# Kernel tuning notes

Measured on AMD Instinct MI355X. Metric: run time of the kernel, lower is better.

## Reference

```python
import jax, jax.numpy as jnp
import numpy as np

N_NODES = 50000
N_EDGES = 800000
F_IN = 128
HID = 128
N_CLASSES = 12
N_GRAPHS = 128


def setup_inputs() -> dict:
    key = jax.random.key(0)
    ks = jax.random.split(key, 12)
    x = jax.random.normal(ks[0], (N_NODES, F_IN), dtype=jnp.float32)
    edge_index = jax.random.randint(ks[1], (2, N_EDGES), 0, N_NODES, dtype=jnp.int64)
    batch = jnp.sort(jax.random.randint(ks[2], (N_NODES,), 0, N_GRAPHS, dtype=jnp.int64))
    def glorot(k, fan_in, fan_out):
        s = jnp.sqrt(6.0 / (fan_in + fan_out))
        return jax.random.uniform(k, (fan_in, fan_out), jnp.float32, -s, s)
    return {
        "x": x,
        "edge_index": edge_index,
        "batch": batch,
        "W0": glorot(ks[3], F_IN, HID), "b0": jnp.zeros((HID,), jnp.float32),
        "W1": glorot(ks[4], HID, HID), "b1": jnp.zeros((HID,), jnp.float32),
        "W2": glorot(ks[5], HID, HID), "b2": jnp.zeros((HID,), jnp.float32),
        "lin_w": glorot(ks[6], HID, N_CLASSES),
        "lin_b": jnp.zeros((N_CLASSES,), jnp.float32),
    }


def _gcn_norm(edge_index, n_nodes):
    # add self loops then compute symmetric normalization D^-1/2 (A+I) D^-1/2
    loops = jnp.arange(n_nodes, dtype=edge_index.dtype)
    row = jnp.concatenate([edge_index[0], loops])
    col = jnp.concatenate([edge_index[1], loops])
    deg = jax.ops.segment_sum(jnp.ones_like(col, dtype=jnp.float32), col, num_segments=n_nodes)
    dis = jnp.where(deg > 0, jax.lax.rsqrt(deg), 0.0)
    norm = dis[row] * dis[col]  # [E + N]
    return row, col, norm


def _gcn_conv(x, W, b, row, col, norm, n_nodes):
    xw = x @ W                                   # [N, H] dense GEMM
    msg = xw[row] * norm[:, None]                # gather + scale [E+N, H]
    out = jax.ops.segment_sum(msg, col, num_segments=n_nodes)  # scatter-add
    return out + b


def reference(x, edge_index, batch, W0, b0, W1, b1, W2, b2, lin_w, lin_b):
    n = x.shape[0]
    row, col, norm = _gcn_norm(edge_index, n)
    h = x
    for W, b in ((W0, b0), (W1, b1), (W2, b2)):
        h = jax.nn.relu(_gcn_conv(h, W, b, row, col, norm, n))
        # dropout is identity in eval mode
    # global mean pool over graphs
    sums = jax.ops.segment_sum(h, batch, num_segments=N_GRAPHS)        # [G, H]
    cnt = jax.ops.segment_sum(jnp.ones((n,), h.dtype), batch, num_segments=N_GRAPHS)
    pooled = sums / jnp.maximum(cnt, 1.0)[:, None]
    return pooled @ lin_w + lin_b  # [G, C]
```

## Files before the change

### kernel.cpp

```cpp
#include <hip/hip_runtime.h>
#include <hip/hip_bf16.h>

#define HID 128
#define NCLS 12
#define NGRAPH 128

typedef __attribute__((ext_vector_type(8))) short short8v;
typedef __attribute__((ext_vector_type(4))) float float4v;

__device__ __forceinline__ ushort f2bf(float f) {
    uint u = __float_as_uint(f);
    u += 0x7FFFu + ((u >> 16) & 1u);
    return (ushort)(u >> 16);
}
__device__ __forceinline__ float bf2f(ushort u) {
    return __uint_as_float(((uint)u) << 16);
}
__device__ __forceinline__ float4 bf4tof(ushort4 u) {
    float4 f;
    f.x = bf2f(u.x); f.y = bf2f(u.y); f.z = bf2f(u.z); f.w = bf2f(u.w);
    return f;
}


__global__ void hist_kernel(const int* __restrict__ ei, int* __restrict__ cnt, int E) {
    int e = blockIdx.x * blockDim.x + threadIdx.x;
    if (e < E) {
        int c = ei[E + e];
        atomicAdd(&cnt[c], 1);
    }
}

__global__ void scan1_kernel(const int* __restrict__ cnt, int* __restrict__ offs,
                             int* __restrict__ bsum, float* __restrict__ dis, int n) {
    __shared__ int s[1024];
    int t = threadIdx.x;
    int v = blockIdx.x * 1024 + t;
    int val = (v < n) ? cnt[v] : 0;
    if (v < n) dis[v] = rsqrtf((float)(val + 1));
    s[t] = val;
    __syncthreads();
    for (int off = 1; off < 1024; off <<= 1) {
        int add = (t >= off) ? s[t - off] : 0;
        __syncthreads();
        s[t] += add;
        __syncthreads();
    }
    if (v < n) offs[v] = s[t] - val;
    if (t == 1023) bsum[blockIdx.x] = s[1023];
}

__global__ void scan2_kernel(const int* __restrict__ bsum, int* __restrict__ bscan, int nb) {
    if (threadIdx.x == 0 && blockIdx.x == 0) {
        int run = 0;
        for (int b = 0; b < nb; b++) { bscan[b] = run; run += bsum[b]; }
        bscan[nb] = run;
    }
}

__global__ void scan3_kernel(int* __restrict__ offs, int* __restrict__ cursor,
                             const int* __restrict__ bscan, int n, int E) {
    int v = blockIdx.x * blockDim.x + threadIdx.x;
    if (v < n) {
        int o = offs[v] + bscan[v >> 10];
        offs[v] = o;
        cursor[v] = o;
    }
    if (v == 0) offs[n] = E;
}

__global__ void fill_kernel(const int* __restrict__ ei, int* __restrict__ cursor,
                            int* __restrict__ srcs, int E) {
    int e = blockIdx.x * blockDim.x + threadIdx.x;
    if (e < E) {
        int r = ei[e];
        int c = ei[E + e];
        int p = atomicAdd(&cursor[c], 1);
        srcs[p] = r;
    }
}


__global__ void cvtx_kernel(const float* __restrict__ x, ushort* __restrict__ xb, int total) {
    int i = (blockIdx.x * blockDim.x + threadIdx.x) * 4;
    if (i < total) {
        float4 v = *(const float4*)&x[i];
        ushort4 o;
        o.x = f2bf(v.x); o.y = f2bf(v.y); o.z = f2bf(v.z); o.w = f2bf(v.w);
        *(ushort4*)&xb[i] = o;
    }
}

__global__ void cvtw_kernel(const float* __restrict__ W, ushort* __restrict__ Wt) {
    int idx = blockIdx.x * 256 + threadIdx.x;
    int k = idx >> 7;
    int c = idx & 127;
    Wt[c * HID + k] = f2bf(W[k * HID + c]);
}


__global__ __launch_bounds__(256) void gemm_bf16_kernel(
    const ushort* __restrict__ A, const ushort* __restrict__ Wt,
    const float* __restrict__ dis, ushort* __restrict__ Y, int n)
{
    int tid  = threadIdx.x;
    int wave = tid >> 6;
    int lane = tid & 63;
    int l15  = lane & 15;
    int lg   = lane >> 4;
    int rowbase = blockIdx.x * 128 + wave * 32;

    float4v acc[2][8];
#pragma unroll
    for (int m = 0; m < 2; m++)
#pragma unroll
        for (int nn = 0; nn < 8; nn++)
            acc[m][nn] = (float4v){0.f, 0.f, 0.f, 0.f};

#pragma unroll
    for (int kk = 0; kk < 4; kk++) {
        int k0 = kk * 32 + lg * 8;
        short8v a[2];
#pragma unroll
        for (int m = 0; m < 2; m++) {
            int row = rowbase + m * 16 + l15;
            if (row < n) a[m] = *(const short8v*)&A[row * HID + k0];
            else         a[m] = (short8v){0,0,0,0,0,0,0,0};
        }
        short8v b[8];
#pragma unroll
        for (int nn = 0; nn < 8; nn++)
            b[nn] = *(const short8v*)&Wt[(nn * 16 + l15) * HID + k0];
#pragma unroll
        for (int m = 0; m < 2; m++)
#pragma unroll
            for (int nn = 0; nn < 8; nn++)
                acc[m][nn] = __builtin_amdgcn_mfma_f32_16x16x32_bf16(
                    b[nn], a[m], acc[m][nn], 0, 0, 0);
    }

#pragma unroll
    for (int m = 0; m < 2; m++) {
        int row = rowbase + m * 16 + l15;
        if (row < n) {
            float d = dis[row];
#pragma unroll
            for (int nn = 0; nn < 8; nn++) {
                ushort4 o;
                o.x = f2bf(acc[m][nn][0] * d);
                o.y = f2bf(acc[m][nn][1] * d);
                o.z = f2bf(acc[m][nn][2] * d);
                o.w = f2bf(acc[m][nn][3] * d);
                *(ushort4*)&Y[row * HID + nn * 16 + lg * 4] = o;
            }
        }
    }
}


__global__ __launch_bounds__(256) void aggregate_bf16_kernel(
    const ushort* __restrict__ Y, const int* __restrict__ offs,
    const int* __restrict__ srcs, const float* __restrict__ dis,
    const float* __restrict__ bias, ushort* __restrict__ H, int n)
{
    int tid = threadIdx.x;
    int node = blockIdx.x * 8 + (tid >> 5);
    if (node >= n) return;
    int lane = tid & 31;
    int c = lane * 4;
    const ushort* Yc = Y + c;

    float4 a0 = bf4tof(*(const ushort4*)&Yc[node * HID]);
    float4 a1 = make_float4(0.f, 0.f, 0.f, 0.f);
    float4 a2 = make_float4(0.f, 0.f, 0.f, 0.f);
    float4 a3 = make_float4(0.f, 0.f, 0.f, 0.f);
    float4 a4 = make_float4(0.f, 0.f, 0.f, 0.f);
    float4 a5 = make_float4(0.f, 0.f, 0.f, 0.f);
    float4 a6 = make_float4(0.f, 0.f, 0.f, 0.f);
    float4 a7 = make_float4(0.f, 0.f, 0.f, 0.f);

    int beg = offs[node];
    int end = offs[node + 1];
    int j = beg;
    for (; j + 8 <= end; j += 8) {
        int r0 = srcs[j + 0], r1 = srcs[j + 1], r2 = srcs[j + 2], r3 = srcs[j + 3];
        int r4 = srcs[j + 4], r5 = srcs[j + 5], r6 = srcs[j + 6], r7 = srcs[j + 7];
        float4 v0 = bf4tof(*(const ushort4*)&Yc[r0 * HID]);
        float4 v1 = bf4tof(*(const ushort4*)&Yc[r1 * HID]);
        float4 v2 = bf4tof(*(const ushort4*)&Yc[r2 * HID]);
        float4 v3 = bf4tof(*(const ushort4*)&Yc[r3 * HID]);
        float4 v4 = bf4tof(*(const ushort4*)&Yc[r4 * HID]);
        float4 v5 = bf4tof(*(const ushort4*)&Yc[r5 * HID]);
        float4 v6 = bf4tof(*(const ushort4*)&Yc[r6 * HID]);
        float4 v7 = bf4tof(*(const ushort4*)&Yc[r7 * HID]);
        a0.x += v0.x; a0.y += v0.y; a0.z += v0.z; a0.w += v0.w;
        a1.x += v1.x; a1.y += v1.y; a1.z += v1.z; a1.w += v1.w;
        a2.x += v2.x; a2.y += v2.y; a2.z += v2.z; a2.w += v2.w;
        a3.x += v3.x; a3.y += v3.y; a3.z += v3.z; a3.w += v3.w;
        a4.x += v4.x; a4.y += v4.y; a4.z += v4.z; a4.w += v4.w;
        a5.x += v5.x; a5.y += v5.y; a5.z += v5.z; a5.w += v5.w;
        a6.x += v6.x; a6.y += v6.y; a6.z += v6.z; a6.w += v6.w;
        a7.x += v7.x; a7.y += v7.y; a7.z += v7.z; a7.w += v7.w;
    }
    for (; j + 2 <= end; j += 2) {
        int r0 = srcs[j + 0], r1 = srcs[j + 1];
        float4 v0 = bf4tof(*(const ushort4*)&Yc[r0 * HID]);
        float4 v1 = bf4tof(*(const ushort4*)&Yc[r1 * HID]);
        a0.x += v0.x; a0.y += v0.y; a0.z += v0.z; a0.w += v0.w;
        a1.x += v1.x; a1.y += v1.y; a1.z += v1.z; a1.w += v1.w;
    }
    if (j < end) {
        int r0 = srcs[j];
        float4 v0 = bf4tof(*(const ushort4*)&Yc[r0 * HID]);
        a0.x += v0.x; a0.y += v0.y; a0.z += v0.z; a0.w += v0.w;
    }

    a0.x += a1.x + a2.x + a3.x + a4.x + a5.x + a6.x + a7.x;
    a0.y += a1.y + a2.y + a3.y + a4.y + a5.y + a6.y + a7.y;
    a0.z += a1.z + a2.z + a3.z + a4.z + a5.z + a6.z + a7.z;
    a0.w += a1.w + a2.w + a3.w + a4.w + a5.w + a6.w + a7.w;

    float d = dis[node];
    float4 bb = *(const float4*)&bias[c];
    ushort4 o;
    o.x = f2bf(fmaxf(fmaf(d, a0.x, bb.x), 0.f));
    o.y = f2bf(fmaxf(fmaf(d, a0.y, bb.y), 0.f));
    o.z = f2bf(fmaxf(fmaf(d, a0.z, bb.z), 0.f));
    o.w = f2bf(fmaxf(fmaf(d, a0.w, bb.w), 0.f));
    *(ushort4*)&H[node * HID + c] = o;
}


__global__ __launch_bounds__(256) void pool_kernel(
    const ushort* __restrict__ H, const int* __restrict__ batch,
    float* __restrict__ gsum, float* __restrict__ gcnt, int n)
{
    int half = blockIdx.x * 8 + (threadIdx.x >> 5);
    int lane = threadIdx.x & 31;
    int c = lane * 4;
    int n0 = half * 16;
    if (n0 >= n) return;
    int n1 = min(n0 + 16, n);

    float4 acc = make_float4(0.f, 0.f, 0.f, 0.f);
    float cntv = 0.f;
    int gprev = batch[n0];
    for (int v = n0; v < n1; v++) {
        int g = batch[v];
        if (g != gprev) {
            atomicAdd(&gsum[gprev * HID + c + 0], acc.x);
            atomicAdd(&gsum[gprev * HID + c + 1], acc.y);
            atomicAdd(&gsum[gprev * HID + c + 2], acc.z);
            atomicAdd(&gsum[gprev * HID + c + 3], acc.w);
            if (lane == 0) atomicAdd(&gcnt[gprev], cntv);
            acc = make_float4(0.f, 0.f, 0.f, 0.f);
            cntv = 0.f;
            gprev = g;
        }
        float4 h = bf4tof(*(const ushort4*)&H[v * HID + c]);
        acc.x += h.x; acc.y += h.y; acc.z += h.z; acc.w += h.w;
        cntv += 1.f;
    }
    atomicAdd(&gsum[gprev * HID + c + 0], acc.x);
    atomicAdd(&gsum[gprev * HID + c + 1], acc.y);
    atomicAdd(&gsum[gprev * HID + c + 2], acc.z);
    atomicAdd(&gsum[gprev * HID + c + 3], acc.w);
    if (lane == 0) atomicAdd(&gcnt[gprev], cntv);
}


__global__ __launch_bounds__(128) void classify_kernel(
    const float* __restrict__ gsum, const float* __restrict__ gcnt,
    const float* __restrict__ lin_w, const float* __restrict__ lin_b,
    float* __restrict__ out)
{
    __shared__ float sp[HID];
    int g = blockIdx.x;
    int f = threadIdx.x;
    float denom = fmaxf(gcnt[g], 1.0f);
    sp[f] = gsum[g * HID + f] / denom;
    __syncthreads();
    if (f < NCLS) {
        float acc = lin_b[f];
        for (int k = 0; k < HID; k++) acc = fmaf(sp[k], lin_w[k * NCLS + f], acc);
        out[g * NCLS + f] = acc;
    }
}


extern "C" void kernel_launch(void* const* d_in, const int* in_sizes, int n_in,
                              void* d_out, int out_size, void* d_ws, size_t ws_size,
                              hipStream_t stream) {
    const float* x     = (const float*)d_in[0];
    const int*   ei    = (const int*)d_in[1];
    const int*   batch = (const int*)d_in[2];
    const float* W0    = (const float*)d_in[3];
    const float* b0    = (const float*)d_in[4];
    const float* W1    = (const float*)d_in[5];
    const float* b1    = (const float*)d_in[6];
    const float* W2    = (const float*)d_in[7];
    const float* b2    = (const float*)d_in[8];
    const float* lin_w = (const float*)d_in[9];
    const float* lin_b = (const float*)d_in[10];
    float* out = (float*)d_out;

    const int n = in_sizes[0] / HID;
    const int E = in_sizes[1] / 2;

    char* w = (char*)d_ws;
    auto carve = [&](size_t bytes) {
        void* p = (void*)w;
        w += (bytes + 255) & ~(size_t)255;
        return p;
    };
    int*    cnt    = (int*)carve((size_t)n * 4);
    int*    offs   = (int*)carve(((size_t)n + 1) * 4);
    int*    cursor = (int*)carve((size_t)n * 4);
    int*    bsum   = (int*)carve(256 * 4);
    int*    bscan  = (int*)carve(256 * 4);
    int*    srcs   = (int*)carve((size_t)E * 4);
    float*  dis    = (float*)carve((size_t)n * 4);
    ushort* xb     = (ushort*)carve((size_t)n * HID * 2);
    ushort* Wt0    = (ushort*)carve((size_t)HID * HID * 2);
    ushort* Wt1    = (ushort*)carve((size_t)HID * HID * 2);
    ushort* Wt2    = (ushort*)carve((size_t)HID * HID * 2);
    ushort* Y      = (ushort*)carve((size_t)n * HID * 2);
    ushort* Hb     = (ushort*)carve((size_t)n * HID * 2);
    float*  gsum   = (float*)carve((size_t)NGRAPH * HID * 4);
    float*  gcnt   = (float*)carve((size_t)NGRAPH * 4);

    hipMemsetAsync(cnt, 0, (size_t)n * 4, stream);
    hipMemsetAsync(gsum, 0, (size_t)NGRAPH * HID * 4, stream);
    hipMemsetAsync(gcnt, 0, (size_t)NGRAPH * 4, stream);

    const int TB = 256;
    int gE = (E + TB - 1) / TB;
    int gN = (n + TB - 1) / TB;
    int nb1 = (n + 1023) / 1024;

    hist_kernel<<<gE, TB, 0, stream>>>(ei, cnt, E);
    scan1_kernel<<<nb1, 1024, 0, stream>>>(cnt, offs, bsum, dis, n);
    scan2_kernel<<<1, 64, 0, stream>>>(bsum, bscan, nb1);
    scan3_kernel<<<gN, TB, 0, stream>>>(offs, cursor, bscan, n, E);
    fill_kernel<<<gE, TB, 0, stream>>>(ei, cursor, srcs, E);

    int totalx = n * HID;
    cvtx_kernel<<<(totalx / 4 + TB - 1) / TB, TB, 0, stream>>>(x, xb, totalx);
    cvtw_kernel<<<64, 256, 0, stream>>>(W0, Wt0);
    cvtw_kernel<<<64, 256, 0, stream>>>(W1, Wt1);
    cvtw_kernel<<<64, 256, 0, stream>>>(W2, Wt2);

    int gGemm = (n + 127) / 128;
    int gAgg  = (n + 7) / 8;

    gemm_bf16_kernel<<<gGemm, TB, 0, stream>>>(xb, Wt0, dis, Y, n);
    aggregate_bf16_kernel<<<gAgg, TB, 0, stream>>>(Y, offs, srcs, dis, b0, Hb, n);
    gemm_bf16_kernel<<<gGemm, TB, 0, stream>>>(Hb, Wt1, dis, Y, n);
    aggregate_bf16_kernel<<<gAgg, TB, 0, stream>>>(Y, offs, srcs, dis, b1, Hb, n);
    gemm_bf16_kernel<<<gGemm, TB, 0, stream>>>(Hb, Wt2, dis, Y, n);
    aggregate_bf16_kernel<<<gAgg, TB, 0, stream>>>(Y, offs, srcs, dis, b2, Hb, n);

    int halves = (n + 15) / 16;
    int gPool = (halves + 7) / 8;
    pool_kernel<<<gPool, TB, 0, stream>>>(Hb, batch, gsum, gcnt, n);
    classify_kernel<<<NGRAPH, 128, 0, stream>>>(gsum, gcnt, lin_w, lin_b, out);
}
```

Measured before the change: 377.0 us.

## Build CSR via two-level bucket partition with shared-memory atomics

Replaces the five-kernel CSR build (global atomic histogram, three scan kernels, global atomic fill) with three kernels. Edges are first bucketed by destination block (256 nodes) per 4096-edge section in shared memory, then each block counts and places its own edges with shared-memory atomics. This removes heavy global atomic contention and several launches, at the cost of an intermediate int2 partition buffer. In csr_kernel each thread walks one section serially, so load balance depends on how edges are spread across sections, and edge order within a node changes.

```diff
diff --git a/kernel.cpp b/kernel.cpp
--- a/kernel.cpp
+++ b/kernel.cpp
@@ -4,6 +4,7 @@
 #define HID 128
 #define NCLS 12
 #define NGRAPH 128
+#define EPB 4096
 
 typedef __attribute__((ext_vector_type(8))) short short8v;
 typedef __attribute__((ext_vector_type(4))) float float4v;
@@ -23,60 +24,114 @@
 }
 
 
-__global__ void hist_kernel(const int* __restrict__ ei, int* __restrict__ cnt, int E) {
-    int e = blockIdx.x * blockDim.x + threadIdx.x;
-    if (e < E) {
-        int c = ei[E + e];
-        atomicAdd(&cnt[c], 1);
-    }
-}
-
-__global__ void scan1_kernel(const int* __restrict__ cnt, int* __restrict__ offs,
-                             int* __restrict__ bsum, float* __restrict__ dis, int n) {
-    __shared__ int s[1024];
+__global__ __launch_bounds__(256) void part_kernel(
+    const int* __restrict__ ei, int2* __restrict__ part,
+    int* __restrict__ lscan, int* __restrict__ btot, int E, int nb)
+{
+    __shared__ int h[256], sc[256], cur[256];
+    int k = blockIdx.x;
     int t = threadIdx.x;
-    int v = blockIdx.x * 1024 + t;
-    int val = (v < n) ? cnt[v] : 0;
-    if (v < n) dis[v] = rsqrtf((float)(val + 1));
-    s[t] = val;
-    __syncthreads();
-    for (int off = 1; off < 1024; off <<= 1) {
-        int add = (t >= off) ? s[t - off] : 0;
-        __syncthreads();
-        s[t] += add;
-        __syncthreads();
-    }
-    if (v < n) offs[v] = s[t] - val;
-    if (t == 1023) bsum[blockIdx.x] = s[1023];
-}
-
-__global__ void scan2_kernel(const int* __restrict__ bsum, int* __restrict__ bscan, int nb) {
-    if (threadIdx.x == 0 && blockIdx.x == 0) {
-        int run = 0;
-        for (int b = 0; b < nb; b++) { bscan[b] = run; run += bsum[b]; }
-        bscan[nb] = run;
-    }
-}
-
-__global__ void scan3_kernel(int* __restrict__ offs, int* __restrict__ cursor,
-                             const int* __restrict__ bscan, int n, int E) {
-    int v = blockIdx.x * blockDim.x + threadIdx.x;
-    if (v < n) {
-        int o = offs[v] + bscan[v >> 10];
-        offs[v] = o;
-        cursor[v] = o;
-    }
-    if (v == 0) offs[n] = E;
-}
-
-__global__ void fill_kernel(const int* __restrict__ ei, int* __restrict__ cursor,
-                            int* __restrict__ srcs, int E) {
-    int e = blockIdx.x * blockDim.x + threadIdx.x;
-    if (e < E) {
-        int r = ei[e];
-        int c = ei[E + e];
-        int p = atomicAdd(&cursor[c], 1);
-        srcs[p] = r;
+    int e0 = k * EPB, e1 = min(e0 + EPB, E);
+
+    h[t] = 0;
+    __syncthreads();
+    for (int e = e0 + t; e < e1; e += 256)
+        atomicAdd(&h[ei[E + e] >> 8], 1);
+    __syncthreads();
+
+    sc[t] = h[t];
+    __syncthreads();
+    for (int off = 1; off < 256; off <<= 1) {
+        int add = (t >= off) ? sc[t - off] : 0;
+        __syncthreads();
+        sc[t] += add;
+        __syncthreads();
+    }
+    int excl = sc[t] - h[t];
+    cur[t] = excl;
+    if (t < nb) {
+        lscan[k * (nb + 1) + t] = excl;
+        if (h[t] > 0) atomicAdd(&btot[t], h[t]);
+    }
+    if (t == 0) lscan[k * (nb + 1) + nb] = e1 - e0;
+    __syncthreads();
+
+    for (int e = e0 + t; e < e1; e += 256) {
+        int r = ei[e], c = ei[E + e];
+        int lr = atomicAdd(&cur[c >> 8], 1);
+        part[e0 + lr] = make_int2(r, c);
+    }
+}
+
+
+__global__ void gscan_kernel(const int* __restrict__ btot, int* __restrict__ gstart,
+                             int nb, int E) {
+    __shared__ int sc[256];
+    int t = threadIdx.x;
+    int v = (t < nb) ? btot[t] : 0;
+    sc[t] = v;
+    __syncthreads();
+    for (int off = 1; off < 256; off <<= 1) {
+        int add = (t >= off) ? sc[t - off] : 0;
+        __syncthreads();
+        sc[t] += add;
+        __syncthreads();
+    }
+    if (t < nb) gstart[t] = sc[t] - v;
+    if (t == 0) gstart[nb] = E;
+}
+
+
+__global__ __launch_bounds__(256) void csr_kernel(
+    const int2* __restrict__ part, const int* __restrict__ lscan,
+    const int* __restrict__ gstart, int* __restrict__ offs,
+    int* __restrict__ srcs, float* __restrict__ dis,
+    int n, int E, int nb, int nsec)
+{
+    __shared__ int cnt[256], sc[256], cur[256];
+    int b = blockIdx.x, t = threadIdx.x;
+
+    cnt[t] = 0;
+    __syncthreads();
+    for (int k = t; k < nsec; k += 256) {
+        const int* lrow = &lscan[k * (nb + 1)];
+        int s0 = lrow[b], s1 = lrow[b + 1];
+        int base = k * EPB;
+        for (int e = s0; e < s1; e++) {
+            int2 pr = part[base + e];
+            atomicAdd(&cnt[pr.y & 255], 1);
+        }
+    }
+    __syncthreads();
+
+    sc[t] = cnt[t];
+    __syncthreads();
+    for (int off = 1; off < 256; off <<= 1) {
+        int add = (t >= off) ? sc[t - off] : 0;
+        __syncthreads();
+        sc[t] += add;
+        __syncthreads();
+    }
+    int excl = sc[t] - cnt[t];
+    int g0 = gstart[b];
+    int d = b * 256 + t;
+    if (d < n) {
+        offs[d] = g0 + excl;
+        dis[d] = rsqrtf((float)(cnt[t] + 1));
+    }
+    cur[t] = g0 + excl;
+    if (b == nb - 1 && t == 0) offs[n] = E;
+    __syncthreads();
+
+    for (int k = t; k < nsec; k += 256) {
+        const int* lrow = &lscan[k * (nb + 1)];
+        int s0 = lrow[b], s1 = lrow[b + 1];
+        int base = k * EPB;
+        for (int e = s0; e < s1; e++) {
+            int2 pr = part[base + e];
+            int p = atomicAdd(&cur[pr.y & 255], 1);
+            srcs[p] = pr.x;
+        }
     }
 }
 
@@ -306,6 +361,8 @@
 
     const int n = in_sizes[0] / HID;
     const int E = in_sizes[1] / 2;
+    const int nb = (n + 255) / 256;
+    const int nsec = (E + EPB - 1) / EPB;
 
     char* w = (char*)d_ws;
     auto carve = [&](size_t bytes) {
@@ -313,11 +370,11 @@
         w += (bytes + 255) & ~(size_t)255;
         return p;
     };
-    int*    cnt    = (int*)carve((size_t)n * 4);
+    int2*   part   = (int2*)carve((size_t)E * 8);
+    int*    lscan  = (int*)carve((size_t)nsec * (nb + 1) * 4);
+    int*    btot   = (int*)carve((size_t)nb * 4);
+    int*    gstart = (int*)carve((size_t)(nb + 1) * 4);
     int*    offs   = (int*)carve(((size_t)n + 1) * 4);
-    int*    cursor = (int*)carve((size_t)n * 4);
-    int*    bsum   = (int*)carve(256 * 4);
-    int*    bscan  = (int*)carve(256 * 4);
     int*    srcs   = (int*)carve((size_t)E * 4);
     float*  dis    = (float*)carve((size_t)n * 4);
     ushort* xb     = (ushort*)carve((size_t)n * HID * 2);
@@ -329,20 +386,15 @@
     float*  gsum   = (float*)carve((size_t)NGRAPH * HID * 4);
     float*  gcnt   = (float*)carve((size_t)NGRAPH * 4);
 
-    hipMemsetAsync(cnt, 0, (size_t)n * 4, stream);
+    hipMemsetAsync(btot, 0, (size_t)nb * 4, stream);
     hipMemsetAsync(gsum, 0, (size_t)NGRAPH * HID * 4, stream);
     hipMemsetAsync(gcnt, 0, (size_t)NGRAPH * 4, stream);
 
     const int TB = 256;
-    int gE = (E + TB - 1) / TB;
-    int gN = (n + TB - 1) / TB;
-    int nb1 = (n + 1023) / 1024;
-
-    hist_kernel<<<gE, TB, 0, stream>>>(ei, cnt, E);
-    scan1_kernel<<<nb1, 1024, 0, stream>>>(cnt, offs, bsum, dis, n);
-    scan2_kernel<<<1, 64, 0, stream>>>(bsum, bscan, nb1);
-    scan3_kernel<<<gN, TB, 0, stream>>>(offs, cursor, bscan, n, E);
-    fill_kernel<<<gE, TB, 0, stream>>>(ei, cursor, srcs, E);
+
+    part_kernel<<<nsec, TB, 0, stream>>>(ei, part, lscan, btot, E, nb);
+    gscan_kernel<<<1, TB, 0, stream>>>(btot, gstart, nb, E);
+    csr_kernel<<<nb, TB, 0, stream>>>(part, lscan, gstart, offs, srcs, dis, n, E, nb, nsec);
 
     int totalx = n * HID;
     cvtx_kernel<<<(totalx / 4 + TB - 1) / TB, TB, 0, stream>>>(x, xb, totalx);
```

Result: faster. 325.2 us (-13.7%).
